# Performance work log

Measured on AMD Instinct MI355X. Metric: run time of the kernel, lower is better.

Reference implementation:

```python
import jax, jax.numpy as jnp
import numpy as np


def hilbert_perm(M: int) -> np.ndarray:
    """Permutation ordering the first M cells of a Hilbert curve on a 2^k x 2^k grid."""
    side = 1
    while side * side < M:
        side *= 2
    idx = np.arange(M)
    x = (idx % side).astype(np.int64)
    y = (idx // side).astype(np.int64)
    d = np.zeros(M, dtype=np.int64)
    s = side // 2
    while s > 0:
        rx = ((x & s) > 0).astype(np.int64)
        ry = ((y & s) > 0).astype(np.int64)
        d += s * s * ((3 * rx) ^ ry)
        swap = ry == 0
        flip = swap & (rx == 1)
        x2 = np.where(flip, s - 1 - x, x)
        y2 = np.where(flip, s - 1 - y, y)
        x, y = np.where(swap, y2, x2), np.where(swap, x2, y2)
        s //= 2
    return np.argsort(d, kind='stable')


SEGMENT_SIZE = 512


def setup_inputs() -> dict:
    key = jax.random.key(0)
    ks = jax.random.split(key, 5)
    B, M, H, D = 2, 8192, 8, 64
    hd = H * D  # 512
    q = jax.random.normal(ks[0], (B, M, H, D), dtype=jnp.float32)
    k = jax.random.normal(ks[1], (B, M, H, D), dtype=jnp.float32)
    v = jax.random.normal(ks[2], (B, M, H, D), dtype=jnp.float32)
    w_qkv = jax.random.normal(ks[3], (3 * hd, hd), dtype=jnp.float32) * (hd ** -0.5)
    w_out = jax.random.normal(ks[4], (hd, hd), dtype=jnp.float32) * (hd ** -0.5)
    return {"q": q, "k": k, "v": v, "w_qkv": w_qkv, "w_out": w_out}


def reference(q, k, v, w_qkv, w_out):
    B, M, H, D = q.shape
    hd = H * D
    S = SEGMENT_SIZE
    n_seg = M // S
    # Wrapper: mean over heads, then channel-repeat to hidden_dim
    x = q.mean(axis=2)                       # [B, M, D]
    x = jnp.tile(x, (1, 1, H))               # [B, M, hd]
    # HilbertAttentionCore: fused QKV projection
    qkv = jnp.einsum('bmc,fc->bmf', x, w_qkv)  # [B, M, 3*hd]
    qh, kh, vh = jnp.split(qkv, 3, axis=-1)
    # Hilbert-curve reordering (static permutation of seq dim)
    perm = jnp.asarray(hilbert_perm(M))
    inv = jnp.argsort(perm)
    def seg(t):
        t = t[:, perm]                       # reorder seq
        return t.reshape(B, n_seg, S, H, D)
    qs, ks_, vs = seg(qh), seg(kh), seg(vh)
    scale = D ** -0.5
    scores = jnp.einsum('bnshd,bnthd->bnhst', qs, ks_) * scale  # [B,n_seg,H,S,S]
    attn = jax.nn.softmax(scores, axis=-1)
    out = jnp.einsum('bnhst,bnthd->bnshd', attn, vs)            # [B,n_seg,S,H,D]
    out = out.reshape(B, M, hd)[:, inv]      # undo Hilbert ordering
    out = jnp.einsum('bmc,fc->bmf', out, w_out)  # output projection
    return out.reshape(B, M, H, D)
```

## Files before the change

### kernel.cpp

```cpp
#include <hip/hip_runtime.h>


typedef short bfrag __attribute__((ext_vector_type(8)));
typedef float ffrag __attribute__((ext_vector_type(4)));
typedef short svec4 __attribute__((ext_vector_type(4)));
typedef unsigned uvec4 __attribute__((ext_vector_type(4)));

__device__ inline short f2bf(float x) {
  unsigned u = __builtin_bit_cast(unsigned, x);
  u = (u + 0x7fffu + ((u >> 16) & 1u)) >> 16;
  return (short)u;
}
__device__ inline unsigned pk2f(float a, float b) {
  unsigned ua = (__builtin_bit_cast(unsigned, a) + 0x8000u) >> 16;
  unsigned ub = __builtin_bit_cast(unsigned, b) + 0x8000u;
  return ua | (ub & 0xffff0000u);
}
__device__ inline float fexp2(float x) {
#if __has_builtin(__builtin_amdgcn_exp2f)
  return __builtin_amdgcn_exp2f(x);
#else
  return __expf(x * 0.6931471805599453f);
#endif
}
__device__ inline void gload_lds16(const void* g, void* l) {
  __builtin_amdgcn_global_load_lds(
      (const __attribute__((address_space(1))) unsigned*)g,
      (__attribute__((address_space(3))) unsigned*)l, 16, 0, 0);
}

__device__ inline int d2xy128(int d) {
  int x = 0, y = 0, t = d;
  for (int s = 1; s < 128; s <<= 1) {
    int rx = 1 & (t >> 1);
    int ry = 1 & (t ^ rx);
    if (ry == 0) {
      if (rx == 1) { x = s - 1 - x; y = s - 1 - y; }
      int tt = x; x = y; y = tt;
    }
    x += s * rx;
    y += s * ry;
    t >>= 2;
  }
  return y * 128 + x;
}

__global__ __launch_bounds__(256) void prep_kernel(
    const float* __restrict__ q, const float* __restrict__ w_qkv,
    const float* __restrict__ w_out, short* __restrict__ xmean,
    short* __restrict__ weff, short* __restrict__ woutb,
    int* __restrict__ perm) {
  int i = blockIdx.x * 256 + threadIdx.x;
  if (i < 1048576) {
    int bm = i >> 6, d = i & 63;
    const float* p = q + (size_t)bm * 512 + d;
    float s = 0.f;
#pragma unroll
    for (int h = 0; h < 8; ++h) s += p[h * 64];
    xmean[i] = f2bf(s * 0.125f);
  } else if (i < 1048576 + 98304) {
    int j = i - 1048576;
    int f = j >> 6;
    const float* p = w_qkv + (size_t)f * 512 + (j & 63);
    float s = 0.f;
#pragma unroll
    for (int r = 0; r < 8; ++r) s += p[r * 64];
    if (f < 512) s *= 0.125f * 1.44269504088896f;
    weff[j] = f2bf(s);
  } else if (i < 1048576 + 98304 + 262144) {
    int j = i - 1048576 - 98304;
    woutb[j] = f2bf(w_out[j]);
  } else if (i < 1048576 + 98304 + 262144 + 8192) {
    int r = i - (1048576 + 98304 + 262144);
    perm[r] = d2xy128(r < 4096 ? r : r + 8192);
  }
}

__global__ __launch_bounds__(256) void qkv_kernel(
    const short* __restrict__ xmean, const short* __restrict__ weff,
    const int* __restrict__ perm, short* __restrict__ Qs,
    short* __restrict__ Ks, short* __restrict__ Vt) {
  int tid = threadIdx.x;
  int w = tid >> 6, lane = tid & 63;
  int ml = lane & 15, quad = lane >> 4;
  int rg = blockIdx.x >> 2, fq = blockIdx.x & 3;
  int r0 = rg * 64 + w * 16;
  int r = r0 + ml;
  int b = r >> 13, p = r & 8191;
  int src = (b << 13) + perm[p];
  bfrag a0 = *(const bfrag*)(xmean + (size_t)src * 64 + quad * 8);
  bfrag a1 = *(const bfrag*)(xmean + (size_t)src * 64 + 32 + quad * 8);
  int p0 = r0 & 8191;
  int bq = r0 >> 13;
  int nseg = p0 >> 9;
  int sbase = (p0 & 511) + quad * 4;

  auto loadW = [&](bfrag (&wf)[2], int nt) {
    const short* wp = weff + (size_t)(nt * 16 + ml) * 64 + quad * 8;
    wf[0] = *(const bfrag*)(wp);
    wf[1] = *(const bfrag*)(wp + 32);
  };
  auto emit = [&](bfrag (&wf)[2], int nt) {
    int f0 = nt * 16;
    ffrag acc = {0.f, 0.f, 0.f, 0.f};
    if (f0 < 1024) {
      acc = __builtin_amdgcn_mfma_f32_16x16x32_bf16(wf[0], a0, acc, 0, 0, 0);
      acc = __builtin_amdgcn_mfma_f32_16x16x32_bf16(wf[1], a1, acc, 0, 0, 0);
      short* dst = (f0 < 512) ? Qs : Ks;
      svec4 pk;
#pragma unroll
      for (int g = 0; g < 4; ++g) pk[g] = f2bf(acc[g]);
      *(svec4*)(dst + (size_t)(r0 + ml) * 512 + (f0 & 511) + quad * 4) = pk;
    } else {
      acc = __builtin_amdgcn_mfma_f32_16x16x32_bf16(a0, wf[0], acc, 0, 0, 0);
      acc = __builtin_amdgcn_mfma_f32_16x16x32_bf16(a1, wf[1], acc, 0, 0, 0);
      int fl = f0 + ml - 1024;
      int hh = fl >> 6, dd = fl & 63;
      svec4 pk;
#pragma unroll
      for (int g = 0; g < 4; ++g) pk[g] = f2bf(acc[g]);
      *(svec4*)(Vt + ((((size_t)bq * 16 + nseg) * 8 + hh) * 64 + dd) * 512 +
                sbase) = pk;
    }
  };

  int base = fq * 24;
  bfrag wA[2], wB[2];
  loadW(wA, base);
#pragma unroll 1
  for (int it = 0; it < 12; ++it) {
    int nt0 = base + it * 2;
    loadW(wB, nt0 + 1);
    emit(wA, nt0);
    loadW(wA, (it < 11) ? nt0 + 2 : base);
    emit(wB, nt0 + 1);
  }
}

__global__ __launch_bounds__(256, 2) void attn_kernel(
    const short* __restrict__ Qs, const short* __restrict__ Ks,
    const short* __restrict__ Vt, const int* __restrict__ perm,
    short* __restrict__ aout) {
  __shared__ short Klds[2][32 * 64];
  __shared__ short Vlds[2][64 * 32];
  int tid = threadIdx.x;
  int w = tid >> 6, lane = tid & 63;
  int ml = lane & 15, quad = lane >> 4;
  int sh = blockIdx.x & 255;
  int qq = blockIdx.x >> 8;
  int b = sh >> 7;
  int n = (sh >> 3) & 15;
  int h = sh & 7;
  size_t segrow = (size_t)(b * 8192 + n * 512);
  const short* Qseg = Qs + segrow * 512 + h * 64;
  const short* Kseg = Ks + segrow * 512 + h * 64;
  const short* Vseg = Vt + (((size_t)(b * 16 + n) * 8 + h) * 64) * 512;
  int q0 = qq * 256 + w * 64;
  bfrag qa[4][2];
#pragma unroll
  for (int nq = 0; nq < 4; ++nq)
#pragma unroll
    for (int ks = 0; ks < 2; ++ks)
      qa[nq][ks] = *(const bfrag*)(Qseg + (size_t)(q0 + nq * 16 + ml) * 512 +
                                   ks * 32 + quad * 8);
  ffrag o[4][4];
  float lrun[4] = {0.f, 0.f, 0.f, 0.f};
#pragma unroll
  for (int nq = 0; nq < 4; ++nq)
#pragma unroll
    for (int dt = 0; dt < 4; ++dt) o[nq][dt] = (ffrag){0.f, 0.f, 0.f, 0.f};

  int lA = (((quad & 1) << 5) + ml) << 2;
  int lB = lA + 64;
  bool hi = quad >= 2;

  int krow = lane >> 3;
  int kug = (lane & 7) ^ krow;
  int vrow = w * 16 + (lane >> 2);
  int vug = (lane & 3) ^ ((lane >> 3) & 3);

  auto stage = [&](int buf, int t0) {
    gload_lds16(Kseg + (size_t)(t0 + w * 8 + krow) * 512 + kug * 8,
                (char*)&Klds[buf][0] + w * 1024);
    gload_lds16(Vseg + (size_t)vrow * 512 + t0 + vug * 8,
                (char*)&Vlds[buf][0] + w * 1024);
  };

  auto body = [&](int buf) {
    const char* Kb = (const char*)&Klds[buf][0];
    const char* Vb = (const char*)&Vlds[buf][0];
    bfrag kk[2][2], vv[4];
#pragma unroll
    for (int mt = 0; mt < 2; ++mt)
#pragma unroll
      for (int ks = 0; ks < 2; ++ks) {
        int row = mt * 16 + ml;
        int byte = row * 128 + ks * 64 + quad * 16;
        kk[mt][ks] = *(const bfrag*)(Kb + (byte ^ ((row & 7) << 4)));
      }
#pragma unroll
    for (int dt = 0; dt < 4; ++dt) {
      int row = dt * 16 + ml;
      int byte = row * 64 + quad * 16;
      vv[dt] = *(const bfrag*)(Vb + (byte ^ (((row >> 1) & 3) << 4)));
    }
#pragma unroll
    for (int nq = 0; nq < 4; ++nq) {
      ffrag c0 = {0.f, 0.f, 0.f, 0.f}, c1 = {0.f, 0.f, 0.f, 0.f};
      c0 = __builtin_amdgcn_mfma_f32_16x16x32_bf16(kk[0][0], qa[nq][0], c0, 0, 0, 0);
      c0 = __builtin_amdgcn_mfma_f32_16x16x32_bf16(kk[0][1], qa[nq][1], c0, 0, 0, 0);
      c1 = __builtin_amdgcn_mfma_f32_16x16x32_bf16(kk[1][0], qa[nq][0], c1, 0, 0, 0);
      c1 = __builtin_amdgcn_mfma_f32_16x16x32_bf16(kk[1][1], qa[nq][1], c1, 0, 0, 0);
      float e0 = fexp2(c0[0]), e1 = fexp2(c0[1]);
      float e2 = fexp2(c0[2]), e3 = fexp2(c0[3]);
      float e4 = fexp2(c1[0]), e5 = fexp2(c1[1]);
      float e6 = fexp2(c1[2]), e7 = fexp2(c1[3]);
      lrun[nq] += ((e0 + e1) + (e2 + e3)) + ((e4 + e5) + (e6 + e7));
      unsigned P0 = pk2f(e0, e1), P1 = pk2f(e2, e3);
      unsigned P2 = pk2f(e4, e5), P3 = pk2f(e6, e7);
      unsigned r0 = __builtin_amdgcn_ds_bpermute(lA, (int)P0);
      unsigned r1 = __builtin_amdgcn_ds_bpermute(lA, (int)P1);
      unsigned r2 = __builtin_amdgcn_ds_bpermute(lB, (int)P0);
      unsigned r3 = __builtin_amdgcn_ds_bpermute(lB, (int)P1);
      unsigned r4 = __builtin_amdgcn_ds_bpermute(lA, (int)P2);
      unsigned r5 = __builtin_amdgcn_ds_bpermute(lA, (int)P3);
      unsigned r6 = __builtin_amdgcn_ds_bpermute(lB, (int)P2);
      unsigned r7 = __builtin_amdgcn_ds_bpermute(lB, (int)P3);
      uvec4 pu;
      pu[0] = hi ? r4 : r0;
      pu[1] = hi ? r5 : r1;
      pu[2] = hi ? r6 : r2;
      pu[3] = hi ? r7 : r3;
      bfrag pa = __builtin_bit_cast(bfrag, pu);
#pragma unroll
      for (int dt = 0; dt < 4; ++dt)
        o[nq][dt] = __builtin_amdgcn_mfma_f32_16x16x32_bf16(vv[dt], pa,
                                                            o[nq][dt], 0, 0, 0);
    }
  };

  stage(0, 0);
  __syncthreads();
  int cur = 0;
#pragma unroll 1
  for (int jj = 0; jj < 15; ++jj) {
    stage(cur ^ 1, (jj + 1) * 32);
    body(cur);
    __syncthreads();
    cur ^= 1;
  }
  body(cur);

#pragma unroll
  for (int nq = 0; nq < 4; ++nq) {
    float l = lrun[nq];
    l += __shfl_xor(l, 16);
    l += __shfl_xor(l, 32);
    float inv = 1.f / l;
    int sout = q0 + nq * 16 + ml;
    int om = perm[n * 512 + sout];
    size_t base = ((size_t)(b * 8192 + om)) * 512 + h * 64;
#pragma unroll
    for (int dt = 0; dt < 4; ++dt) {
      svec4 pk;
#pragma unroll
      for (int g = 0; g < 4; ++g) pk[g] = f2bf(o[nq][dt][g] * inv);
      *(svec4*)(aout + base + dt * 16 + quad * 4) = pk;
    }
  }
}

__global__ __launch_bounds__(256, 2) void proj_kernel(
    const short* __restrict__ aout, const short* __restrict__ woutb,
    float* __restrict__ out) {
  __shared__ short As[2][128 * 64];
  __shared__ short Bs[2][128 * 64];
  int tid = threadIdx.x;
  int w = tid >> 6, lane = tid & 63;
  int ml = lane & 15, quad = lane >> 4;
  int rb = blockIdx.x & 127;
  int cb = blockIdx.x >> 7;
  int r0 = rb * 128, c0 = cb * 128;
  int wr = (w >> 1) * 64, wc = (w & 1) * 64;

  ffrag acc[4][4];
#pragma unroll
  for (int m = 0; m < 4; ++m)
#pragma unroll
    for (int n = 0; n < 4; ++n) acc[m][n] = (ffrag){0.f, 0.f, 0.f, 0.f};

  int srow = w * 32 + (lane >> 3);
  int scol = (lane & 7) * 8;
  const short* gA = aout + (size_t)(r0 + srow) * 512 + scol;
  const short* gB = woutb + (size_t)(c0 + srow) * 512 + scol;

  auto stage = [&](int buf, int k0) {
#pragma unroll
    for (int i = 0; i < 4; ++i) {
      gload_lds16(gA + (size_t)i * 8 * 512 + k0,
                  (char*)&As[buf][0] + w * 4096 + i * 1024);
      gload_lds16(gB + (size_t)i * 8 * 512 + k0,
                  (char*)&Bs[buf][0] + w * 4096 + i * 1024);
    }
  };
  auto compute = [&](int buf) {
#pragma unroll
    for (int kk = 0; kk < 2; ++kk) {
      bfrag af[4], bf[4];
#pragma unroll
      for (int m = 0; m < 4; ++m)
        af[m] = *(const bfrag*)&As[buf][(wr + m * 16 + ml) * 64 + kk * 32 +
                                        quad * 8];
#pragma unroll
      for (int n = 0; n < 4; ++n)
        bf[n] = *(const bfrag*)&Bs[buf][(wc + n * 16 + ml) * 64 + kk * 32 +
                                        quad * 8];
#pragma unroll
      for (int m = 0; m < 4; ++m)
#pragma unroll
        for (int n = 0; n < 4; ++n)
          acc[m][n] = __builtin_amdgcn_mfma_f32_16x16x32_bf16(bf[n], af[m],
                                                              acc[m][n], 0, 0, 0);
    }
  };

  stage(0, 0);
  __syncthreads();
  int cur = 0;
#pragma unroll 1
  for (int t = 0; t < 7; ++t) {
    stage(cur ^ 1, (t + 1) * 64);
    compute(cur);
    __syncthreads();
    cur ^= 1;
  }
  compute(cur);

#pragma unroll
  for (int m = 0; m < 4; ++m)
#pragma unroll
    for (int n = 0; n < 4; ++n)
      *(ffrag*)(out + (size_t)(r0 + wr + m * 16 + ml) * 512 + c0 + wc +
                n * 16 + quad * 4) = acc[m][n];
}

extern "C" void kernel_launch(void* const* d_in, const int* in_sizes, int n_in,
                              void* d_out, int out_size, void* d_ws,
                              size_t ws_size, hipStream_t stream) {
  const float* q = (const float*)d_in[0];
  const float* w_qkv = (const float*)d_in[3];
  const float* w_out = (const float*)d_in[4];
  float* out = (float*)d_out;

  char* ws = (char*)d_ws;
  int* perm = (int*)ws;
  short* xmean = (short*)(ws + 32768);
  short* weff = (short*)(ws + 2129920);
  short* woutb = (short*)(ws + 2326528);
  short* Qs = (short*)(ws + 2850816);
  short* Ks = (short*)(ws + 19628032);
  short* Vt = (short*)(ws + 36405248);
  short* aout = (short*)(ws + 53182464);

  prep_kernel<<<5536, 256, 0, stream>>>(q, w_qkv, w_out, xmean, weff, woutb,
                                        perm);
  qkv_kernel<<<1024, 256, 0, stream>>>(xmean, weff, perm, Qs, Ks, Vt);
  attn_kernel<<<512, 256, 0, stream>>>(Qs, Ks, Vt, perm, aout);
  proj_kernel<<<512, 256, 0, stream>>>(aout, woutb, out);
}
```

Measured before the change: 203.9 us.

## Stage QKV weights in LDS and coalesce Q/K stores via shared staging

The QKV projection kernel now copies its 384-row weight slice into swizzled LDS once per block using direct global-to-LDS loads, instead of each wave streaming weight fragments from global memory per tile. For the Q and K outputs, results are first written to a per-wave LDS staging buffer and then written out as full 16-byte row vectors, replacing the scattered 8-byte stores. This is meant to cut redundant global weight traffic and improve store coalescing. In exchange it uses about 66 KB of LDS per block and adds a block-wide barrier, and the launch bounds now request two blocks per CU.

```diff
diff --git a/kernel.cpp b/kernel.cpp
--- a/kernel.cpp
+++ b/kernel.cpp
@@ -76,10 +76,12 @@
   }
 }
 
-__global__ __launch_bounds__(256) void qkv_kernel(
+__global__ __launch_bounds__(256, 2) void qkv_kernel(
     const short* __restrict__ xmean, const short* __restrict__ weff,
     const int* __restrict__ perm, short* __restrict__ Qs,
     short* __restrict__ Ks, short* __restrict__ Vt) {
+  __shared__ short Wlds[384 * 64];
+  __shared__ short Sb[4][2][16 * 72];
   int tid = threadIdx.x;
   int w = tid >> 6, lane = tid & 63;
   int ml = lane & 15, quad = lane >> 4;
@@ -95,45 +97,69 @@
   int nseg = p0 >> 9;
   int sbase = (p0 & 511) + quad * 4;
 
-  auto loadW = [&](bfrag (&wf)[2], int nt) {
-    const short* wp = weff + (size_t)(nt * 16 + ml) * 64 + quad * 8;
-    wf[0] = *(const bfrag*)(wp);
-    wf[1] = *(const bfrag*)(wp + 32);
-  };
-  auto emit = [&](bfrag (&wf)[2], int nt) {
-    int f0 = nt * 16;
-    ffrag acc = {0.f, 0.f, 0.f, 0.f};
-    if (f0 < 1024) {
-      acc = __builtin_amdgcn_mfma_f32_16x16x32_bf16(wf[0], a0, acc, 0, 0, 0);
-      acc = __builtin_amdgcn_mfma_f32_16x16x32_bf16(wf[1], a1, acc, 0, 0, 0);
-      short* dst = (f0 < 512) ? Qs : Ks;
-      svec4 pk;
-#pragma unroll
-      for (int g = 0; g < 4; ++g) pk[g] = f2bf(acc[g]);
-      *(svec4*)(dst + (size_t)(r0 + ml) * 512 + (f0 & 511) + quad * 4) = pk;
+  {
+    int lrow = lane >> 3;
+    int lu = lane & 7;
+    const short* wsrc = weff + (size_t)(fq * 384 + w * 96 + lrow) * 64 +
+                        ((lu ^ (lrow & 7)) * 8);
+#pragma unroll
+    for (int i = 0; i < 12; ++i)
+      gload_lds16(wsrc + (size_t)i * 8 * 64,
+                  (char*)Wlds + w * 12288 + i * 1024);
+  }
+  __syncthreads();
+
+#pragma unroll 1
+  for (int gg = 0; gg < 6; ++gg) {
+    int nt0 = fq * 24 + gg * 4;
+    int f0g = nt0 * 16;
+    short* sb = &Sb[w][gg & 1][0];
+    if (f0g < 1024) {
+#pragma unroll
+      for (int t = 0; t < 4; ++t) {
+        int row = (gg * 4 + t) * 16 + ml;
+        const char* Wb = (const char*)Wlds + row * 128;
+        int sw = (row & 7) << 4;
+        bfrag wf0 = *(const bfrag*)(Wb + ((quad << 4) ^ sw));
+        bfrag wf1 = *(const bfrag*)(Wb + (((4 + quad) << 4) ^ sw));
+        ffrag acc = {0.f, 0.f, 0.f, 0.f};
+        acc = __builtin_amdgcn_mfma_f32_16x16x32_bf16(wf0, a0, acc, 0, 0, 0);
+        acc = __builtin_amdgcn_mfma_f32_16x16x32_bf16(wf1, a1, acc, 0, 0, 0);
+        svec4 pk;
+#pragma unroll
+        for (int g = 0; g < 4; ++g) pk[g] = f2bf(acc[g]);
+        *(svec4*)((char*)sb + ml * 144 + t * 32 + quad * 8) = pk;
+      }
+      __builtin_amdgcn_sched_barrier(0);
+      int rrow = lane >> 3;
+      int cu = lane & 7;
+      bfrag v0 = *(const bfrag*)((char*)sb + rrow * 144 + cu * 16);
+      bfrag v1 = *(const bfrag*)((char*)sb + (rrow + 8) * 144 + cu * 16);
+      short* dst = (f0g < 512) ? Qs : Ks;
+      int fo = f0g & 511;
+      *(bfrag*)(dst + (size_t)(r0 + rrow) * 512 + fo + cu * 8) = v0;
+      *(bfrag*)(dst + (size_t)(r0 + rrow + 8) * 512 + fo + cu * 8) = v1;
     } else {
-      acc = __builtin_amdgcn_mfma_f32_16x16x32_bf16(a0, wf[0], acc, 0, 0, 0);
-      acc = __builtin_amdgcn_mfma_f32_16x16x32_bf16(a1, wf[1], acc, 0, 0, 0);
-      int fl = f0 + ml - 1024;
-      int hh = fl >> 6, dd = fl & 63;
-      svec4 pk;
-#pragma unroll
-      for (int g = 0; g < 4; ++g) pk[g] = f2bf(acc[g]);
-      *(svec4*)(Vt + ((((size_t)bq * 16 + nseg) * 8 + hh) * 64 + dd) * 512 +
-                sbase) = pk;
-    }
-  };
-
-  int base = fq * 24;
-  bfrag wA[2], wB[2];
-  loadW(wA, base);
-#pragma unroll 1
-  for (int it = 0; it < 12; ++it) {
-    int nt0 = base + it * 2;
-    loadW(wB, nt0 + 1);
-    emit(wA, nt0);
-    loadW(wA, (it < 11) ? nt0 + 2 : base);
-    emit(wB, nt0 + 1);
+#pragma unroll
+      for (int t = 0; t < 4; ++t) {
+        int nt = nt0 + t;
+        int row = (gg * 4 + t) * 16 + ml;
+        const char* Wb = (const char*)Wlds + row * 128;
+        int sw = (row & 7) << 4;
+        bfrag wf0 = *(const bfrag*)(Wb + ((quad << 4) ^ sw));
+        bfrag wf1 = *(const bfrag*)(Wb + (((4 + quad) << 4) ^ sw));
+        ffrag acc = {0.f, 0.f, 0.f, 0.f};
+        acc = __builtin_amdgcn_mfma_f32_16x16x32_bf16(a0, wf0, acc, 0, 0, 0);
+        acc = __builtin_amdgcn_mfma_f32_16x16x32_bf16(a1, wf1, acc, 0, 0, 0);
+        int fl = nt * 16 + ml - 1024;
+        int hh = fl >> 6, dd = fl & 63;
+        svec4 pk;
+#pragma unroll
+        for (int g = 0; g < 4; ++g) pk[g] = f2bf(acc[g]);
+        *(svec4*)(Vt + ((((size_t)bq * 16 + nseg) * 8 + hh) * 64 + dd) * 512 +
+                  sbase) = pk;
+      }
+    }
   }
 }
 
```

Measured after the change: 192.2 us. -5.7%, faster.
